# Kernel optimization log

Measured on AMD Instinct MI355X. Metric: run time of the kernel, lower is better.

## Reference

```python
import jax, jax.numpy as jnp
import numpy as np
from jax import lax

SOBEL_X = jnp.array([[-1., 0., 1.], [-2., 0., 2.], [-1., 0., 1.]], dtype=jnp.float32)
SOBEL_Y = jnp.array([[-1., -2., -1.], [0., 0., 0.], [1., 2., 1.]], dtype=jnp.float32)


def _extract_boundary(prob):
    # prob: (B, C, H, W). Depthwise 3x3 Sobel conv per channel (one fused grouped conv
    # instead of a Python loop over channels).
    C = prob.shape[1]
    kx = jnp.tile(SOBEL_X.reshape(1, 1, 3, 3), (C, 1, 1, 1))  # (C,1,3,3) OIHW
    ky = jnp.tile(SOBEL_Y.reshape(1, 1, 3, 3), (C, 1, 1, 1))
    dn = ('NCHW', 'OIHW', 'NCHW')
    gx = lax.conv_general_dilated(prob, kx, (1, 1), [(1, 1), (1, 1)],
                                  feature_group_count=C, dimension_numbers=dn)
    gy = lax.conv_general_dilated(prob, ky, (1, 1), [(1, 1), (1, 1)],
                                  feature_group_count=C, dimension_numbers=dn)
    return jnp.sqrt(gx * gx + gy * gy)


def setup_inputs() -> dict:
    key = jax.random.key(0)
    k1, k2 = jax.random.split(key)
    B, C, H, W = 4, 19, 512, 1024
    student_logits = jax.random.normal(k1, (B, C, H, W), dtype=jnp.float32)
    teacher_logits = jax.random.normal(k2, (B, C, H, W), dtype=jnp.float32)
    return {"student_logits": student_logits, "teacher_logits": teacher_logits}


def reference(student_logits, teacher_logits):
    student_prob = jax.nn.softmax(student_logits, axis=1)
    teacher_prob = jax.nn.softmax(teacher_logits, axis=1)
    student_boundary = _extract_boundary(student_prob)
    teacher_boundary = _extract_boundary(teacher_prob)
    diff = student_boundary - teacher_boundary
    return jnp.mean(diff * diff)
```

## Files before the change

kernel.cpp:

```cpp
#include <hip/hip_runtime.h>

#define NB 4
#define NC 19
#define NH 512
#define NW 1024
#define HW (NH * NW)
#define CHW (NC * HW)

#define TW 32
#define TH 8
#define HALO_W (TW + 2)
#define HALO_H (TH + 2)
#define NPX (HALO_W * HALO_H)

__launch_bounds__(256, 3)
__global__ void bdl_fused_kernel(const float* __restrict__ s_logits,
                                 const float* __restrict__ t_logits,
                                 float* __restrict__ out) {
    __shared__ float sprob[2][NC][HALO_H][HALO_W];

    const int tid = threadIdx.x;
    const int h0 = blockIdx.y * TH;
    const int w0 = blockIdx.x * TW;
    const int b  = blockIdx.z;

    for (int idx = tid; idx < NPX; idx += 256) {
        const int py = idx / HALO_W;
        const int px = idx - py * HALO_W;
        const int h = h0 + py - 1;
        const int w = w0 + px - 1;
        const bool inb = (h >= 0) && (h < NH) && (w >= 0) && (w < NW);

        #pragma unroll
        for (int t = 0; t < 2; ++t) {
            const float* __restrict__ src = (t == 0) ? s_logits : t_logits;
            if (inb) {
                const float* __restrict__ p =
                    src + (size_t)b * CHW + (size_t)h * NW + (size_t)w;
                float v[NC];
                float m = -1e30f;
                #pragma unroll
                for (int c = 0; c < NC; ++c) {
                    v[c] = p[(size_t)c * HW];
                    m = fmaxf(m, v[c]);
                }
                float sum = 0.f;
                #pragma unroll
                for (int c = 0; c < NC; ++c) {
                    v[c] = __expf(v[c] - m);
                    sum += v[c];
                }
                const float r = 1.0f / sum;
                #pragma unroll
                for (int c = 0; c < NC; ++c)
                    sprob[t][c][py][px] = v[c] * r;
            } else {
                #pragma unroll
                for (int c = 0; c < NC; ++c)
                    sprob[t][c][py][px] = 0.f;
            }
        }
    }
    __syncthreads();

    const int tx = tid & 31;
    const int ty = tid >> 5;
    float acc = 0.f;

    #pragma unroll 1
    for (int c = 0; c < NC; ++c) {
        float bnd[2];
        #pragma unroll
        for (int t = 0; t < 2; ++t) {
            const float p00 = sprob[t][c][ty    ][tx    ];
            const float p01 = sprob[t][c][ty    ][tx + 1];
            const float p02 = sprob[t][c][ty    ][tx + 2];
            const float p10 = sprob[t][c][ty + 1][tx    ];
            const float p12 = sprob[t][c][ty + 1][tx + 2];
            const float p20 = sprob[t][c][ty + 2][tx    ];
            const float p21 = sprob[t][c][ty + 2][tx + 1];
            const float p22 = sprob[t][c][ty + 2][tx + 2];
            const float gx = (p02 - p00) + 2.f * (p12 - p10) + (p22 - p20);
            const float gy = (p20 - p00) + 2.f * (p21 - p01) + (p22 - p02);
            bnd[t] = sqrtf(fmaf(gx, gx, gy * gy));
        }
        const float d = bnd[0] - bnd[1];
        acc = fmaf(d, d, acc);
    }

    #pragma unroll
    for (int off = 32; off > 0; off >>= 1)
        acc += __shfl_down(acc, off, 64);

    __shared__ float wsum[4];
    if ((tid & 63) == 0) wsum[tid >> 6] = acc;
    __syncthreads();
    if (tid == 0) {
        const float s = wsum[0] + wsum[1] + wsum[2] + wsum[3];
        atomicAdd(out, s * (1.0f / (float)((size_t)NB * NC * NH * NW)));
    }
}

extern "C" void kernel_launch(void* const* d_in, const int* in_sizes, int n_in,
                              void* d_out, int out_size, void* d_ws, size_t ws_size,
                              hipStream_t stream) {
    const float* s_logits = (const float*)d_in[0];
    const float* t_logits = (const float*)d_in[1];
    float* out = (float*)d_out;

    hipMemsetAsync(out, 0, sizeof(float), stream);

    dim3 grid(NW / TW, NH / TH, NB);
    bdl_fused_kernel<<<grid, 256, 0, stream>>>(s_logits, t_logits, out);
}
```

Baseline: 387.8 us.

## Replace shared-memory halo tiles with register sliding window and lane shuffles

Result: slower. 1.387 ms (+257.7%).

```diff
diff --git a/kernel.cpp b/kernel.cpp
--- a/kernel.cpp
+++ b/kernel.cpp
@@ -7,98 +7,106 @@
 #define HW (NH * NW)
 #define CHW (NC * HW)
 
-#define TW 32
-#define TH 8
-#define HALO_W (TW + 2)
-#define HALO_H (TH + 2)
-#define NPX (HALO_W * HALO_H)
+#define STRIP 62
+#define NSTRIP 17
+#define RCH 12
+#define BLKY 11
 
-__launch_bounds__(256, 3)
-__global__ void bdl_fused_kernel(const float* __restrict__ s_logits,
-                                 const float* __restrict__ t_logits,
-                                 float* __restrict__ out) {
-    __shared__ float sprob[2][NC][HALO_H][HALO_W];
+__device__ __forceinline__ void softmax19(float x[NC], float p[NC], bool rv) {
+    float s = 0.f;
+    #pragma unroll
+    for (int c = 0; c < NC; ++c) { x[c] = __expf(x[c]); s += x[c]; }
+    const float r = rv ? __builtin_amdgcn_rcpf(s) : 0.f;
+    #pragma unroll
+    for (int c = 0; c < NC; ++c) p[c] = x[c] * r;
+}
 
-    const int tid = threadIdx.x;
-    const int h0 = blockIdx.y * TH;
-    const int w0 = blockIdx.x * TW;
-    const int b  = blockIdx.z;
+__device__ __forceinline__ float bmag(float pm, float pc, float pp, int lm, int lp) {
+    const float pLm = __shfl(pm, lm, 64), pRm = __shfl(pm, lp, 64);
+    const float pLc = __shfl(pc, lm, 64), pRc = __shfl(pc, lp, 64);
+    const float pLp = __shfl(pp, lm, 64), pRp = __shfl(pp, lp, 64);
+    const float gx = (pRm - pLm) + 2.f * (pRc - pLc) + (pRp - pLp);
+    const float gy = (pLp + 2.f * pp + pRp) - (pLm + 2.f * pm + pRm);
+    return sqrtf(fmaf(gx, gx, gy * gy));
+}
 
-    for (int idx = tid; idx < NPX; idx += 256) {
-        const int py = idx / HALO_W;
-        const int px = idx - py * HALO_W;
-        const int h = h0 + py - 1;
-        const int w = w0 + px - 1;
-        const bool inb = (h >= 0) && (h < NH) && (w >= 0) && (w < NW);
+__launch_bounds__(256, 2)
+__global__ void bdl_kernel(const float* __restrict__ S, const float* __restrict__ T,
+                           float* __restrict__ out) {
+    const int tid  = threadIdx.x;
+    const int lane = tid & 63;
+    const int wv   = tid >> 6;
+    const int lm = lane - 1, lp = lane + 1;
 
+    const int col  = blockIdx.x * STRIP - 1 + lane;
+    const int colc = min(max(col, 0), NW - 1);
+    const bool col_in = (col >= 0) && (col < NW);
+    const bool out_ok = (lane >= 1) && (lane <= STRIP) && col_in;
+
+    const int r0 = (blockIdx.y * 4 + wv) * RCH;
+    const float* __restrict__ Sb = S + (size_t)blockIdx.z * CHW;
+    const float* __restrict__ Tb = T + (size_t)blockIdx.z * CHW;
+
+    float ps[3][NC], pt[3][NC];
+
+    #pragma unroll
+    for (int k = 0; k < 3; ++k) {
+        const int row  = r0 - 1 + k;
+        const int rowc = min(max(row, 0), NH - 1);
+        const int off  = rowc * NW + colc;
+        float xs[NC], xt[NC];
         #pragma unroll
-        for (int t = 0; t < 2; ++t) {
-            const float* __restrict__ src = (t == 0) ? s_logits : t_logits;
-            if (inb) {
-                const float* __restrict__ p =
-                    src + (size_t)b * CHW + (size_t)h * NW + (size_t)w;
-                float v[NC];
-                float m = -1e30f;
-                #pragma unroll
-                for (int c = 0; c < NC; ++c) {
-                    v[c] = p[(size_t)c * HW];
-                    m = fmaxf(m, v[c]);
-                }
-                float sum = 0.f;
-                #pragma unroll
-                for (int c = 0; c < NC; ++c) {
-                    v[c] = __expf(v[c] - m);
-                    sum += v[c];
-                }
-                const float r = 1.0f / sum;
-                #pragma unroll
-                for (int c = 0; c < NC; ++c)
-                    sprob[t][c][py][px] = v[c] * r;
-            } else {
-                #pragma unroll
-                for (int c = 0; c < NC; ++c)
-                    sprob[t][c][py][px] = 0.f;
-            }
-        }
+        for (int c = 0; c < NC; ++c) { xs[c] = Sb[c * HW + off]; xt[c] = Tb[c * HW + off]; }
+        const bool rv = col_in && (row >= 0) && (row < NH);
+        softmax19(xs, ps[k], rv);
+        softmax19(xt, pt[k], rv);
     }
-    __syncthreads();
 
-    const int tx = tid & 31;
-    const int ty = tid >> 5;
     float acc = 0.f;
 
-    #pragma unroll 1
-    for (int c = 0; c < NC; ++c) {
-        float bnd[2];
-        #pragma unroll
-        for (int t = 0; t < 2; ++t) {
-            const float p00 = sprob[t][c][ty    ][tx    ];
-            const float p01 = sprob[t][c][ty    ][tx + 1];
-            const float p02 = sprob[t][c][ty    ][tx + 2];
-            const float p10 = sprob[t][c][ty + 1][tx    ];
-            const float p12 = sprob[t][c][ty + 1][tx + 2];
-            const float p20 = sprob[t][c][ty + 2][tx    ];
-            const float p21 = sprob[t][c][ty + 2][tx + 1];
-            const float p22 = sprob[t][c][ty + 2][tx + 2];
-            const float gx = (p02 - p00) + 2.f * (p12 - p10) + (p22 - p20);
-            const float gy = (p20 - p00) + 2.f * (p21 - p01) + (p22 - p02);
-            bnd[t] = sqrtf(fmaf(gx, gx, gy * gy));
-        }
-        const float d = bnd[0] - bnd[1];
-        acc = fmaf(d, d, acc);
+#define BODY(K, IA, IB, IC, PRE_EXPR)                                                   \
+    {                                                                                   \
+        const int r = r0 + g * 3 + (K);                                                 \
+        float xs[NC], xt[NC];                                                           \
+        const bool pre = (PRE_EXPR);                                                    \
+        if (pre) {                                                                      \
+            const int rowc = min(r + 2, NH - 1);                                        \
+            const int off  = rowc * NW + colc;                                          \
+            _Pragma("unroll")                                                           \
+            for (int c = 0; c < NC; ++c) { xs[c] = Sb[c * HW + off];                    \
+                                           xt[c] = Tb[c * HW + off]; }                  \
+        }                                                                               \
+        float racc = 0.f;                                                               \
+        _Pragma("unroll")                                                               \
+        for (int c = 0; c < NC; ++c) {                                                  \
+            const float bs = bmag(ps[IA][c], ps[IB][c], ps[IC][c], lm, lp);             \
+            const float bt = bmag(pt[IA][c], pt[IB][c], pt[IC][c], lm, lp);             \
+            const float d  = bs - bt;                                                   \
+            racc = fmaf(d, d, racc);                                                    \
+        }                                                                               \
+        acc += (out_ok && (r < NH)) ? racc : 0.f;                                       \
+        if (pre) {                                                                      \
+            const bool rv = col_in && (r + 2 < NH);                                     \
+            softmax19(xs, ps[IA], rv);                                                  \
+            softmax19(xt, pt[IA], rv);                                                  \
+        }                                                                               \
     }
 
+    for (int g = 0; g < 4; ++g) {
+        BODY(0, 0, 1, 2, 1)
+        BODY(1, 1, 2, 0, 1)
+        BODY(2, 2, 0, 1, g < 3)
+    }
+#undef BODY
+
     #pragma unroll
-    for (int off = 32; off > 0; off >>= 1)
-        acc += __shfl_down(acc, off, 64);
-
+    for (int o = 32; o > 0; o >>= 1) acc += __shfl_down(acc, o, 64);
     __shared__ float wsum[4];
-    if ((tid & 63) == 0) wsum[tid >> 6] = acc;
+    if (lane == 0) wsum[wv] = acc;
     __syncthreads();
-    if (tid == 0) {
-        const float s = wsum[0] + wsum[1] + wsum[2] + wsum[3];
-        atomicAdd(out, s * (1.0f / (float)((size_t)NB * NC * NH * NW)));
-    }
+    if (tid == 0)
+        atomicAdd(out, (wsum[0] + wsum[1] + wsum[2] + wsum[3]) *
+                           (1.f / (float)((size_t)NB * NC * NH * NW)));
 }
 
 extern "C" void kernel_launch(void* const* d_in, const int* in_sizes, int n_in,
@@ -110,6 +118,6 @@
 
     hipMemsetAsync(out, 0, sizeof(float), stream);
 
-    dim3 grid(NW / TW, NH / TH, NB);
-    bdl_fused_kernel<<<grid, 256, 0, stream>>>(s_logits, t_logits, out);
+    dim3 grid(NSTRIP, BLKY, NB);
+    bdl_kernel<<<grid, 256, 0, stream>>>(s_logits, t_logits, out);
 }
```
